# Performance work log

Hardware: AMD Instinct MI355X
Metric: run time of the kernel (lower is better)

Reference implementation:

```python
import jax, jax.numpy as jnp
import numpy as np
from jax import lax

B, L, D_IN, D_H = 4096, 64, 256, 200


def setup_inputs() -> dict:
    key = jax.random.key(0)
    ks = jax.random.split(key, 9)
    s_in = 1.0 / np.sqrt(D_IN)
    s_cv = 1.0 / np.sqrt(D_IN * 4)
    return {
        "x": jax.random.normal(ks[0], (B, L, D_IN), dtype=jnp.float32),
        "Wq": jax.random.uniform(ks[1], (D_H, D_IN), jnp.float32, -s_in, s_in),
        "bq": jax.random.uniform(ks[2], (D_H,), jnp.float32, -s_in, s_in),
        "Wk": jax.random.uniform(ks[3], (D_H, D_IN), jnp.float32, -s_in, s_in),
        "bk": jax.random.uniform(ks[4], (D_H,), jnp.float32, -s_in, s_in),
        "Wv": jax.random.uniform(ks[5], (D_H, D_IN), jnp.float32, -s_in, s_in),
        "bv": jax.random.uniform(ks[6], (D_H,), jnp.float32, -s_in, s_in),
        "conv_w": jax.random.uniform(ks[7], (D_H, D_IN, 4), jnp.float32, -s_cv, s_cv),
        "conv_b": jax.random.uniform(ks[8], (D_H,), jnp.float32, -s_cv, s_cv),
    }


def reference(x, Wq, bq, Wk, bk, Wv, bv, conv_w, conv_b):
    # x: [B, L=64, 256]
    q = jax.nn.relu(jnp.einsum("bld,hd->blh", x, Wq) + bq)  # [B,L,200]
    k = jax.nn.relu(jnp.einsum("bld,hd->blh", x, Wk) + bk)  # relu commutes with permute
    v = jax.nn.relu(jnp.einsum("bld,hd->blh", x, Wv) + bv)
    scores = jnp.einsum("blh,bmh->blm", q, k)               # bmm(q, k^T): [B,L,L]
    soft = jax.nn.softmax(scores, axis=1)                   # NOTE: dim=1 (over queries), as in original
    self_att = jnp.einsum("blm,bmh->blh", soft, v)          # [B,L,200]
    b = x.shape[0]
    self_att = self_att.reshape(b, -1, 4, 16).mean(axis=2).reshape(b, 16, -1)  # [B,16,200]
    word_att = x.reshape(b, 256, 64)                        # [B, C=256, len=64]
    conv = lax.conv_general_dilated(
        word_att, conv_w, window_strides=(4,), padding="VALID",
        dimension_numbers=("NCH", "OIH", "NCH"))            # [B,200,16]
    conv = conv + conv_b[None, :, None]
    conv = conv.reshape(b, 16, -1)                          # raw reshape, as in original
    return conv + self_att                                  # [B,16,200]
```

## Files before the change

kernel.cpp:

```cpp
#include <hip/hip_runtime.h>

typedef _Float16 f16x8 __attribute__((ext_vector_type(8)));
typedef _Float16 f16x4 __attribute__((ext_vector_type(4)));
typedef float f32x4 __attribute__((ext_vector_type(4)));

static __device__ __forceinline__ f32x4 MFMA(f16x8 a, f16x8 b, f32x4 c) {
  return __builtin_amdgcn_mfma_f32_16x16x32_f16(a, b, c, 0, 0, 0);
}

__global__ void wcvt(const float* __restrict__ Wq, const float* __restrict__ Wk,
                     const float* __restrict__ Wv, const float* __restrict__ cw,
                     const float* __restrict__ bq, const float* __restrict__ bk,
                     const float* __restrict__ bv,
                     _Float16* __restrict__ Wb,
                     _Float16* __restrict__ Wcb,
                     float* __restrict__ biasp) {
  int gt = blockIdx.x * blockDim.x + threadIdx.x;
  int gs = gridDim.x * blockDim.x;
  const int WN = 224 * 256;
  for (int i = gt; i < WN; i += gs) {
    int n = i >> 8;
    Wb[i]          = (n < 200) ? (_Float16)Wq[i] : (_Float16)0.f;
    Wb[WN + i]     = (n < 200) ? (_Float16)Wk[i] : (_Float16)0.f;
    Wb[2 * WN + i] = (n < 200) ? (_Float16)Wv[i] : (_Float16)0.f;
  }
  for (int i = gt; i < 224 * 1024; i += gs) {
    int o = i >> 10;
    Wcb[i] = (o < 200) ? (_Float16)cw[i] : (_Float16)0.f;
  }
  for (int i = gt; i < 224; i += gs) {
    biasp[i]       = (i < 200) ? bq[i] : 0.f;
    biasp[224 + i] = (i < 200) ? bk[i] : 0.f;
    biasp[448 + i] = (i < 200) ? bv[i] : 0.f;
  }
}

__global__ __launch_bounds__(512, 4) void k1_proj_conv(
    const float* __restrict__ x, const _Float16* __restrict__ Wb,
    const _Float16* __restrict__ Wcb, const float* __restrict__ biasp,
    const float* __restrict__ convb,
    _Float16* __restrict__ Qg, _Float16* __restrict__ Kg,
    _Float16* __restrict__ Vtg, float* __restrict__ out) {
  extern __shared__ char smem[];
  _Float16* Xl = (_Float16*)smem;
  const int tid = threadIdx.x, lane = tid & 63, wave = tid >> 6;
  const int li = lane & 15, g = lane >> 4;
  const int b0 = blockIdx.x * 2;

  const float* xb = x + (size_t)b0 * 16384;
#pragma unroll
  for (int j = 0; j < 16; j++) {
    int f = tid + 512 * j;
    float4 v = ((const float4*)xb)[f];
    int bt = f >> 12, rem = f & 4095, l = rem >> 6, c4 = rem & 63;
    f16x4 h;
    h.x = (_Float16)v.x; h.y = (_Float16)v.y;
    h.z = (_Float16)v.z; h.w = (_Float16)v.w;
    *(f16x4*)(Xl + bt * 16896 + l * 264 + c4 * 4) = h;
  }
  __syncthreads();

#pragma unroll 1
  for (int i = 0; i < 7; i++) {
    int u = wave + 8 * i;
    if (u < 28) {
      int p = u / 14, nt = u % 14;
      const _Float16* wrow = Wb + p * 57344 + (nt * 16 + li) * 256 + 8 * g;
      f32x4 acc[2][4] = {};
#pragma unroll
      for (int kk = 0; kk < 8; kk++) {
        f16x8 aw = *(const f16x8*)(wrow + 32 * kk);
#pragma unroll
        for (int bt = 0; bt < 2; bt++)
#pragma unroll
          for (int mt = 0; mt < 4; mt++) {
            f16x8 bx = *(const f16x8*)(Xl + bt * 16896 + (mt * 16 + li) * 264 + 32 * kk + 8 * g);
            acc[bt][mt] = MFMA(aw, bx, acc[bt][mt]);
          }
      }
      float4 b4 = *(const float4*)(biasp + p * 224 + nt * 16 + 4 * g);
      _Float16* dst0 = (p == 0) ? Qg : Kg;
#pragma unroll
      for (int bt = 0; bt < 2; bt++) {
        _Float16* db = dst0 + (size_t)(b0 + bt) * 14336;
#pragma unroll
        for (int mt = 0; mt < 4; mt++) {
          f16x4 hv;
          {
            float v0 = acc[bt][mt][0] + b4.x; hv[0] = (_Float16)(v0 > 0.f ? v0 : 0.f);
            float v1 = acc[bt][mt][1] + b4.y; hv[1] = (_Float16)(v1 > 0.f ? v1 : 0.f);
            float v2 = acc[bt][mt][2] + b4.z; hv[2] = (_Float16)(v2 > 0.f ? v2 : 0.f);
            float v3 = acc[bt][mt][3] + b4.w; hv[3] = (_Float16)(v3 > 0.f ? v3 : 0.f);
          }
          *(f16x4*)(db + (mt * 16 + li) * 224 + nt * 16 + 4 * g) = hv;
        }
      }
    } else if (u < 42) {
      int nt = u - 28;
      const _Float16* wrow = Wb + 2 * 57344 + (nt * 16 + li) * 256 + 8 * g;
      f32x4 acc[2][4] = {};
#pragma unroll
      for (int kk = 0; kk < 8; kk++) {
        f16x8 bw = *(const f16x8*)(wrow + 32 * kk);
#pragma unroll
        for (int bt = 0; bt < 2; bt++)
#pragma unroll
          for (int mt = 0; mt < 4; mt++) {
            f16x8 ax = *(const f16x8*)(Xl + bt * 16896 + (mt * 16 + li) * 264 + 32 * kk + 8 * g);
            acc[bt][mt] = MFMA(ax, bw, acc[bt][mt]);
          }
      }
      float bias = biasp[448 + nt * 16 + li];
#pragma unroll
      for (int bt = 0; bt < 2; bt++) {
        _Float16* db = Vtg + (size_t)(b0 + bt) * 14336;
#pragma unroll
        for (int mt = 0; mt < 4; mt++) {
          f16x4 hv;
#pragma unroll
          for (int r = 0; r < 4; r++) {
            float v = acc[bt][mt][r] + bias;
            hv[r] = (_Float16)(v > 0.f ? v : 0.f);
          }
          *(f16x4*)(db + (nt * 16 + li) * 64 + mt * 16 + 4 * g) = hv;
        }
      }
    } else {
      int nt = u - 42, o = nt * 16 + li;
      const _Float16* wrow = Wcb + o * 1024 + 8 * g;
      f32x4 acc[2] = {};
#pragma unroll 4
      for (int kk = 0; kk < 32; kk++) {
        f16x8 bf = *(const f16x8*)(wrow + 32 * kk);
        int i1 = kk * 8 + 2 * g;
        int i2 = i1 + 1;
#pragma unroll
        for (int bt = 0; bt < 2; bt++) {
          const _Float16* xt = Xl + bt * 16896;
          union { f16x4 h[2]; f16x8 v; } af;
          af.h[0] = *(const f16x4*)(xt + (i1 >> 2) * 264 + ((i1 & 3) << 6) + 4 * li);
          af.h[1] = *(const f16x4*)(xt + (i2 >> 2) * 264 + ((i2 & 3) << 6) + 4 * li);
          acc[bt] = MFMA(af.v, bf, acc[bt]);
        }
      }
      if (o < 200) {
        float cb = convb[o];
#pragma unroll
        for (int bt = 0; bt < 2; bt++) {
          float4 vo;
          vo.x = acc[bt][0] + cb; vo.y = acc[bt][1] + cb;
          vo.z = acc[bt][2] + cb; vo.w = acc[bt][3] + cb;
          *(float4*)(out + (size_t)(b0 + bt) * 3200 + o * 16 + 4 * g) = vo;
        }
      }
    }
  }
}

#define K3_LDS 68608
__global__ __launch_bounds__(256, 2) void k3_attn(
    const _Float16* __restrict__ Qg, const _Float16* __restrict__ Kg,
    const _Float16* __restrict__ Vtg, float* __restrict__ out) {
  extern __shared__ char smem[];
  _Float16* Qs = (_Float16*)smem;
  _Float16* Ks = (_Float16*)(smem + 29696);
  float*    Sf = (float*)smem;
  _Float16* Vt = (_Float16*)(smem + 29696);
  _Float16* Sb = (_Float16*)(smem + 59392);
  float*    Po = (float*)smem;

  const int b = blockIdx.x;
  const int tid = threadIdx.x, lane = tid & 63, wave = tid >> 6;
  const int li = lane & 15, g = lane >> 4;
  const size_t bb = (size_t)b * 14336;

#pragma unroll
  for (int i = 0; i < 7; i++) {
    int j = tid + 256 * i;
    f16x8 q = *(const f16x8*)(Qg + bb + j * 8);
    int row = j / 28, col = (j % 28) * 8;
    *(f16x8*)(Qs + row * 232 + col) = q;
  }
#pragma unroll
  for (int i = 0; i < 7; i++) {
    int j = tid + 256 * i;
    f16x8 k = *(const f16x8*)(Kg + bb + j * 8);
    int row = j / 28, col = (j % 28) * 8;
    *(f16x8*)(Ks + row * 232 + col) = k;
  }
  f16x8 vreg[7];
#pragma unroll
  for (int i = 0; i < 7; i++)
    vreg[i] = *(const f16x8*)(Vtg + bb + (tid + 256 * i) * 8);
  __syncthreads();

  f32x4 sacc[4] = {};
  {
    const int mt = wave;
#pragma unroll
    for (int kk = 0; kk < 7; kk++) {
      f16x8 qa = *(const f16x8*)(Qs + (mt * 16 + li) * 232 + kk * 32 + 8 * g);
#pragma unroll
      for (int nt = 0; nt < 4; nt++) {
        f16x8 kb = *(const f16x8*)(Ks + (nt * 16 + li) * 232 + kk * 32 + 8 * g);
        sacc[nt] = MFMA(qa, kb, sacc[nt]);
      }
    }
  }
  __syncthreads();

  {
    const int mt = wave;
#pragma unroll
    for (int nt = 0; nt < 4; nt++)
#pragma unroll
      for (int r = 0; r < 4; r++)
        Sf[(mt * 16 + 4 * g + r) * 65 + nt * 16 + li] = sacc[nt][r];
  }
#pragma unroll
  for (int i = 0; i < 7; i++) {
    int j = tid + 256 * i;
    int h = j >> 3, c = j & 7;
    *(f16x8*)(Vt + h * 64 + ((c ^ (h & 7)) << 3)) = vreg[i];
  }
  __syncthreads();

  {
    int m = tid >> 2, r4 = tid & 3;
    float vals[16], mx = -1e30f;
#pragma unroll
    for (int i2 = 0; i2 < 16; i2++) {
      float v = Sf[(r4 + 4 * i2) * 65 + m];
      vals[i2] = v; mx = fmaxf(mx, v);
    }
    mx = fmaxf(mx, __shfl_xor(mx, 1));
    mx = fmaxf(mx, __shfl_xor(mx, 2));
    float s = 0.f;
#pragma unroll
    for (int i2 = 0; i2 < 16; i2++) { vals[i2] = __expf(vals[i2] - mx); s += vals[i2]; }
    s += __shfl_xor(s, 1);
    s += __shfl_xor(s, 2);
    float inv = 1.f / s;
#pragma unroll
    for (int i2 = 0; i2 < 16; i2++)
      Sb[(r4 + 4 * i2) * 72 + m] = (_Float16)(vals[i2] * inv);
  }
  __syncthreads();

  for (int i = tid; i < 3400; i += 256) ((float*)smem)[i] = 0.f;
  __syncthreads();

  f16x8 pa[2][4];
#pragma unroll
  for (int kk = 0; kk < 2; kk++)
#pragma unroll
    for (int mt = 0; mt < 4; mt++)
      pa[kk][mt] = *(const f16x8*)(Sb + (mt * 16 + li) * 72 + kk * 32 + 8 * g);

  for (int ntl = wave; ntl < 14; ntl += 4) {
    int h = ntl * 16 + li;
    f16x8 vb[2];
#pragma unroll
    for (int kk = 0; kk < 2; kk++) {
      int cm = 4 * kk + g;
      vb[kk] = *(const f16x8*)(Vt + h * 64 + ((cm ^ (h & 7)) << 3));
    }
    f32x4 pacc[4] = {};
#pragma unroll
    for (int kk = 0; kk < 2; kk++)
#pragma unroll
      for (int mt = 0; mt < 4; mt++)
        pacc[mt] = MFMA(pa[kk][mt], vb[kk], pacc[mt]);
    if (h < 200) {
#pragma unroll
      for (int mt = 0; mt < 4; mt++)
#pragma unroll
        for (int r = 0; r < 4; r++) {
          int l = mt * 16 + 4 * g + r;
          int f = l * 200 + h;
          atomicAdd(&Po[(f >> 6) * 17 + (f & 15)], 0.25f * pacc[mt][r]);
        }
    }
  }
  __syncthreads();

  float* ob = out + (size_t)b * 3200;
  for (int t = tid; t < 3200; t += 256) {
    int c = t >> 4;
    ob[t] += Po[c * 17 + (t & 15)];
  }
}

#define FB_LDS 151296
__global__ __launch_bounds__(512, 2) void fused_fallback(
    const float* __restrict__ x, const _Float16* __restrict__ Wb,
    const _Float16* __restrict__ Wcb, const float* __restrict__ biasp,
    const float* __restrict__ convb, float* __restrict__ out) {
  extern __shared__ char smem[];
  _Float16* Xl = (_Float16*)smem;
  _Float16* Qs = (_Float16*)(smem + 33792);
  _Float16* Ks = (_Float16*)(smem + 63488);
  _Float16* Vt = (_Float16*)(smem + 93184);
  float* Sf    = (float*)(smem + 125440);
  _Float16* Sb = (_Float16*)(smem + 142080);
  float* SA    = (float*)(smem + 33792);
  float* Cv    = (float*)(smem + 125440);

  const int b = blockIdx.x;
  const int tid = threadIdx.x;
  const int lane = tid & 63;
  const int wave = tid >> 6;
  const int li = lane & 15;
  const int g = lane >> 4;

  const float* xb = x + (size_t)b * 16384;
  for (int i = tid; i < 4096; i += 512) {
    float4 v = ((const float4*)xb)[i];
    int e = i * 4;
    int l = e >> 8, d = e & 255;
    f16x4 h;
    h.x = (_Float16)v.x; h.y = (_Float16)v.y;
    h.z = (_Float16)v.z; h.w = (_Float16)v.w;
    *(f16x4*)(Xl + l * 264 + d) = h;
  }
  __syncthreads();

  for (int u = wave; u < 42; u += 8) {
    int p = u / 14, nt = u % 14;
    int n = nt * 16 + li;
    const _Float16* wrow = Wb + p * 57344 + n * 256 + 8 * g;
    f16x8 bfr[8];
#pragma unroll
    for (int kk = 0; kk < 8; kk++) bfr[kk] = *(const f16x8*)(wrow + kk * 32);
    float bias = biasp[p * 224 + n];
    for (int m = 0; m < 4; m++) {
      f32x4 acc = {0.f, 0.f, 0.f, 0.f};
      const _Float16* arow = Xl + (m * 16 + li) * 264 + 8 * g;
#pragma unroll
      for (int kk = 0; kk < 8; kk++) acc = MFMA(*(const f16x8*)(arow + kk * 32), bfr[kk], acc);
#pragma unroll
      for (int r = 0; r < 4; r++) {
        int row = m * 16 + 4 * g + r;
        float v = acc[r] + bias;
        v = v > 0.f ? v : 0.f;
        _Float16 hv = (_Float16)v;
        if (p == 0) Qs[row * 232 + n] = hv;
        else if (p == 1) Ks[row * 232 + n] = hv;
        else Vt[n * 72 + row] = hv;
      }
    }
  }
  __syncthreads();

  for (int t = wave * 2; t < wave * 2 + 2; t++) {
    int mt = t >> 2, nt = t & 3;
    f32x4 acc = {0.f, 0.f, 0.f, 0.f};
    const _Float16* qrow = Qs + (mt * 16 + li) * 232 + 8 * g;
    const _Float16* krow = Ks + (nt * 16 + li) * 232 + 8 * g;
#pragma unroll
    for (int kk = 0; kk < 7; kk++)
      acc = MFMA(*(const f16x8*)(qrow + kk * 32), *(const f16x8*)(krow + kk * 32), acc);
#pragma unroll
    for (int r = 0; r < 4; r++)
      Sf[(mt * 16 + 4 * g + r) * 65 + nt * 16 + li] = acc[r];
  }
  __syncthreads();

  {
    int m = tid >> 3, r = tid & 7;
    float vals[8];
    float mx = -1e30f;
#pragma unroll
    for (int i = 0; i < 8; i++) {
      float v = Sf[(r + 8 * i) * 65 + m];
      vals[i] = v;
      mx = fmaxf(mx, v);
    }
    mx = fmaxf(mx, __shfl_xor(mx, 1));
    mx = fmaxf(mx, __shfl_xor(mx, 2));
    mx = fmaxf(mx, __shfl_xor(mx, 4));
    float s = 0.f;
#pragma unroll
    for (int i = 0; i < 8; i++) { vals[i] = __expf(vals[i] - mx); s += vals[i]; }
    s += __shfl_xor(s, 1);
    s += __shfl_xor(s, 2);
    s += __shfl_xor(s, 4);
    float inv = 1.0f / s;
#pragma unroll
    for (int i = 0; i < 8; i++)
      Sb[(r + 8 * i) * 72 + m] = (_Float16)(vals[i] * inv);
  }
  __syncthreads();

  for (int nt = wave; nt < 14; nt += 8) {
    int o = nt * 16 + li;
    const _Float16* wrow = Wcb + o * 1024 + 8 * g;
    f32x4 acc = {0.f, 0.f, 0.f, 0.f};
#pragma unroll 4
    for (int kk = 0; kk < 32; kk++) {
      int i1 = kk * 8 + 2 * g;
      int i2 = i1 + 1;
      union { f16x4 h[2]; f16x8 v; } af;
      af.h[0] = *(const f16x4*)(Xl + (i1 >> 2) * 264 + ((i1 & 3) << 6) + 4 * li);
      af.h[1] = *(const f16x4*)(Xl + (i2 >> 2) * 264 + ((i2 & 3) << 6) + 4 * li);
      acc = MFMA(af.v, *(const f16x8*)(wrow + 32 * kk), acc);
    }
#pragma unroll
    for (int r = 0; r < 4; r++) Cv[(4 * g + r) * 226 + o] = acc[r];
  }

  for (int t = wave; t < 56; t += 8) {
    int mt = t / 14, nt = t % 14;
    f32x4 acc = {0.f, 0.f, 0.f, 0.f};
    const _Float16* arow = Sb + (mt * 16 + li) * 72 + 8 * g;
    const _Float16* brow = Vt + (nt * 16 + li) * 72 + 8 * g;
#pragma unroll
    for (int kk = 0; kk < 2; kk++)
      acc = MFMA(*(const f16x8*)(arow + kk * 32), *(const f16x8*)(brow + kk * 32), acc);
#pragma unroll
    for (int r = 0; r < 4; r++)
      SA[(mt * 16 + 4 * g + r) * 228 + (nt * 16 + li)] = acc[r];
  }
  __syncthreads();

  float* ob = out + (size_t)b * 3200;
  for (int t = tid; t < 3200; t += 512) {
    int c = t >> 4, s = t & 15;
    float cv = Cv[s * 226 + c] + convb[c];
    float pool = 0.f;
#pragma unroll
    for (int j = 0; j < 4; j++) {
      int flat = c * 64 + j * 16 + s;
      int l = flat / 200;
      int h = flat - l * 200;
      pool += SA[l * 228 + h];
    }
    ob[t] = cv + 0.25f * pool;
  }
}

extern "C" void kernel_launch(void* const* d_in, const int* in_sizes, int n_in,
                              void* d_out, int out_size, void* d_ws, size_t ws_size,
                              hipStream_t stream) {
  const float* x  = (const float*)d_in[0];
  const float* Wq = (const float*)d_in[1];
  const float* bq = (const float*)d_in[2];
  const float* Wk = (const float*)d_in[3];
  const float* bk = (const float*)d_in[4];
  const float* Wv = (const float*)d_in[5];
  const float* bv = (const float*)d_in[6];
  const float* cw = (const float*)d_in[7];
  const float* cb = (const float*)d_in[8];

  char* ws = (char*)d_ws;
  _Float16* Wb  = (_Float16*)ws;
  _Float16* Wcb = (_Float16*)(ws + 344064);
  float* biasp  = (float*)(ws + 802816);

  hipLaunchKernelGGL(wcvt, dim3(512), dim3(256), 0, stream,
                     Wq, Wk, Wv, cw, bq, bk, bv, Wb, Wcb, biasp);

  const size_t QKV_BASE = 805888ull;
  const size_t QKV_ONE  = 117440512ull;
  const size_t NEED = QKV_BASE + 3ull * QKV_ONE;

  if (ws_size >= NEED) {
    _Float16* Qg  = (_Float16*)(ws + QKV_BASE);
    _Float16* Kg  = (_Float16*)(ws + QKV_BASE + QKV_ONE);
    _Float16* Vtg = (_Float16*)(ws + QKV_BASE + 2 * QKV_ONE);

    hipFuncSetAttribute((const void*)k1_proj_conv,
                        hipFuncAttributeMaxDynamicSharedMemorySize, 67584);
    hipLaunchKernelGGL(k1_proj_conv, dim3(2048), dim3(512), 67584, stream,
                       x, Wb, Wcb, biasp, cb, Qg, Kg, Vtg, (float*)d_out);

    hipFuncSetAttribute((const void*)k3_attn,
                        hipFuncAttributeMaxDynamicSharedMemorySize, K3_LDS);
    hipLaunchKernelGGL(k3_attn, dim3(4096), dim3(256), K3_LDS, stream,
                       Qg, Kg, Vtg, (float*)d_out);
  } else {
    hipFuncSetAttribute((const void*)fused_fallback,
                        hipFuncAttributeMaxDynamicSharedMemorySize, FB_LDS);
    hipLaunchKernelGGL(fused_fallback, dim3(4096), dim3(512), FB_LDS, stream,
                       x, Wb, Wcb, biasp, cb, (float*)d_out);
  }
}
```

Before: 584.9 us.

## Keep Q and softmax in registers to shrink attention LDS footprint

The attention kernel now loads its Q fragments directly from global memory into registers instead of staging them in LDS. It computes the column softmax on the MFMA accumulators, using cross-lane shuffles plus a small per-wave partials buffer, instead of writing the scores to LDS as fp32 and re-reading them. Po gets its own region and is zeroed at the start, which removes one barrier, and the K row pad shrinks. Together these cut LDS from about 67KB to about 52KB, so launch bounds rise to 3 blocks per CU, at the cost of more registers per thread and extra barriers for the partial reductions.

```diff
diff --git a/kernel.cpp b/kernel.cpp
--- a/kernel.cpp
+++ b/kernel.cpp
@@ -157,105 +157,117 @@
   }
 }
 
-#define K3_LDS 68608
-__global__ __launch_bounds__(256, 2) void k3_attn(
+#define K3_LDS 53024
+__global__ __launch_bounds__(256, 3) void k3_attn(
     const _Float16* __restrict__ Qg, const _Float16* __restrict__ Kg,
     const _Float16* __restrict__ Vtg, float* __restrict__ out) {
   extern __shared__ char smem[];
-  _Float16* Qs = (_Float16*)smem;
-  _Float16* Ks = (_Float16*)(smem + 29696);
-  float*    Sf = (float*)smem;
-  _Float16* Vt = (_Float16*)(smem + 29696);
-  _Float16* Sb = (_Float16*)(smem + 59392);
-  float*    Po = (float*)smem;
+  _Float16* Ks   = (_Float16*)smem;
+  _Float16* Vt   = (_Float16*)smem;
+  _Float16* Sb   = (_Float16*)(smem + 29184);
+  float*    part = (float*)(smem + 38400);
+  float*    Po   = (float*)(smem + 39424);
 
   const int b = blockIdx.x;
   const int tid = threadIdx.x, lane = tid & 63, wave = tid >> 6;
   const int li = lane & 15, g = lane >> 4;
   const size_t bb = (size_t)b * 14336;
-
-#pragma unroll
-  for (int i = 0; i < 7; i++) {
-    int j = tid + 256 * i;
-    f16x8 q = *(const f16x8*)(Qg + bb + j * 8);
-    int row = j / 28, col = (j % 28) * 8;
-    *(f16x8*)(Qs + row * 232 + col) = q;
-  }
+  const int mt = wave;
+
+  for (int i = tid; i < 3400; i += 256) Po[i] = 0.f;
+
 #pragma unroll
   for (int i = 0; i < 7; i++) {
     int j = tid + 256 * i;
     f16x8 k = *(const f16x8*)(Kg + bb + j * 8);
     int row = j / 28, col = (j % 28) * 8;
-    *(f16x8*)(Ks + row * 232 + col) = k;
+    *(f16x8*)(Ks + row * 228 + col) = k;
   }
   f16x8 vreg[7];
 #pragma unroll
   for (int i = 0; i < 7; i++)
     vreg[i] = *(const f16x8*)(Vtg + bb + (tid + 256 * i) * 8);
+  f16x8 qreg[7];
+#pragma unroll
+  for (int kk = 0; kk < 7; kk++)
+    qreg[kk] = *(const f16x8*)(Qg + bb + (mt * 16 + li) * 224 + kk * 32 + 8 * g);
   __syncthreads();
 
   f32x4 sacc[4] = {};
-  {
-    const int mt = wave;
-#pragma unroll
-    for (int kk = 0; kk < 7; kk++) {
-      f16x8 qa = *(const f16x8*)(Qs + (mt * 16 + li) * 232 + kk * 32 + 8 * g);
-#pragma unroll
-      for (int nt = 0; nt < 4; nt++) {
-        f16x8 kb = *(const f16x8*)(Ks + (nt * 16 + li) * 232 + kk * 32 + 8 * g);
-        sacc[nt] = MFMA(qa, kb, sacc[nt]);
-      }
-    }
-  }
-  __syncthreads();
-
-  {
-    const int mt = wave;
-#pragma unroll
-    for (int nt = 0; nt < 4; nt++)
-#pragma unroll
-      for (int r = 0; r < 4; r++)
-        Sf[(mt * 16 + 4 * g + r) * 65 + nt * 16 + li] = sacc[nt][r];
-  }
+#pragma unroll
+  for (int kk = 0; kk < 7; kk++) {
+#pragma unroll
+    for (int nt = 0; nt < 4; nt++) {
+      f16x8 kb = *(const f16x8*)(Ks + (nt * 16 + li) * 228 + kk * 32 + 8 * g);
+      sacc[nt] = MFMA(qreg[kk], kb, sacc[nt]);
+    }
+  }
+  __syncthreads();
+
 #pragma unroll
   for (int i = 0; i < 7; i++) {
     int j = tid + 256 * i;
     int h = j >> 3, c = j & 7;
     *(f16x8*)(Vt + h * 64 + ((c ^ (h & 7)) << 3)) = vreg[i];
   }
-  __syncthreads();
-
+
+  float Mx[4];
   {
-    int m = tid >> 2, r4 = tid & 3;
-    float vals[16], mx = -1e30f;
-#pragma unroll
-    for (int i2 = 0; i2 < 16; i2++) {
-      float v = Sf[(r4 + 4 * i2) * 65 + m];
-      vals[i2] = v; mx = fmaxf(mx, v);
-    }
-    mx = fmaxf(mx, __shfl_xor(mx, 1));
-    mx = fmaxf(mx, __shfl_xor(mx, 2));
-    float s = 0.f;
-#pragma unroll
-    for (int i2 = 0; i2 < 16; i2++) { vals[i2] = __expf(vals[i2] - mx); s += vals[i2]; }
-    s += __shfl_xor(s, 1);
-    s += __shfl_xor(s, 2);
-    float inv = 1.f / s;
-#pragma unroll
-    for (int i2 = 0; i2 < 16; i2++)
-      Sb[(r4 + 4 * i2) * 72 + m] = (_Float16)(vals[i2] * inv);
-  }
-  __syncthreads();
-
-  for (int i = tid; i < 3400; i += 256) ((float*)smem)[i] = 0.f;
+    float mx[4];
+#pragma unroll
+    for (int nt = 0; nt < 4; nt++) {
+      float m0 = fmaxf(fmaxf(sacc[nt][0], sacc[nt][1]), fmaxf(sacc[nt][2], sacc[nt][3]));
+      m0 = fmaxf(m0, __shfl_xor(m0, 16));
+      m0 = fmaxf(m0, __shfl_xor(m0, 32));
+      mx[nt] = m0;
+    }
+    if (g == 0) {
+#pragma unroll
+      for (int nt = 0; nt < 4; nt++) part[mt * 64 + nt * 16 + li] = mx[nt];
+    }
+  }
+  __syncthreads();
+#pragma unroll
+  for (int nt = 0; nt < 4; nt++) {
+    int col = nt * 16 + li;
+    Mx[nt] = fmaxf(fmaxf(part[col], part[64 + col]),
+                   fmaxf(part[128 + col], part[192 + col]));
+  }
+  __syncthreads();
+
+  {
+    float sm[4];
+#pragma unroll
+    for (int nt = 0; nt < 4; nt++) {
+#pragma unroll
+      for (int r = 0; r < 4; r++) sacc[nt][r] = __expf(sacc[nt][r] - Mx[nt]);
+      float s0 = sacc[nt][0] + sacc[nt][1] + sacc[nt][2] + sacc[nt][3];
+      s0 += __shfl_xor(s0, 16);
+      s0 += __shfl_xor(s0, 32);
+      sm[nt] = s0;
+    }
+    if (g == 0) {
+#pragma unroll
+      for (int nt = 0; nt < 4; nt++) part[mt * 64 + nt * 16 + li] = sm[nt];
+    }
+  }
+  __syncthreads();
+#pragma unroll
+  for (int nt = 0; nt < 4; nt++) {
+    int col = nt * 16 + li;
+    float inv = 1.f / (part[col] + part[64 + col] + part[128 + col] + part[192 + col]);
+#pragma unroll
+    for (int r = 0; r < 4; r++)
+      Sb[(mt * 16 + 4 * g + r) * 72 + col] = (_Float16)(sacc[nt][r] * inv);
+  }
   __syncthreads();
 
   f16x8 pa[2][4];
 #pragma unroll
   for (int kk = 0; kk < 2; kk++)
 #pragma unroll
-    for (int mt = 0; mt < 4; mt++)
-      pa[kk][mt] = *(const f16x8*)(Sb + (mt * 16 + li) * 72 + kk * 32 + 8 * g);
+    for (int m2 = 0; m2 < 4; m2++)
+      pa[kk][m2] = *(const f16x8*)(Sb + (m2 * 16 + li) * 72 + kk * 32 + 8 * g);
 
   for (int ntl = wave; ntl < 14; ntl += 4) {
     int h = ntl * 16 + li;
@@ -269,16 +281,16 @@
 #pragma unroll
     for (int kk = 0; kk < 2; kk++)
 #pragma unroll
-      for (int mt = 0; mt < 4; mt++)
-        pacc[mt] = MFMA(pa[kk][mt], vb[kk], pacc[mt]);
+      for (int m2 = 0; m2 < 4; m2++)
+        pacc[m2] = MFMA(pa[kk][m2], vb[kk], pacc[m2]);
     if (h < 200) {
 #pragma unroll
-      for (int mt = 0; mt < 4; mt++)
+      for (int m2 = 0; m2 < 4; m2++)
 #pragma unroll
         for (int r = 0; r < 4; r++) {
-          int l = mt * 16 + 4 * g + r;
+          int l = m2 * 16 + 4 * g + r;
           int f = l * 200 + h;
-          atomicAdd(&Po[(f >> 6) * 17 + (f & 15)], 0.25f * pacc[mt][r]);
+          atomicAdd(&Po[(f >> 6) * 17 + (f & 15)], 0.25f * pacc[m2][r]);
         }
     }
   }
```

Result: slower. 617.6 us (+5.6%).
